# Kernel optimization log

Measured on AMD Instinct MI355X. Metric: run time of the kernel, lower is better.

The kernel has to match this reference:

```python
import jax, jax.numpy as jnp
import numpy as np

B, S, D, H = 8, 1024, 1024, 16
DK = D // H
EPS = 1e-5

def _layernorm(x, w, b):
    mu = jnp.mean(x, axis=-1, keepdims=True)
    var = jnp.mean((x - mu) ** 2, axis=-1, keepdims=True)
    return (x - mu) * jax.lax.rsqrt(var + EPS) * w + b

def setup_inputs() -> dict:
    key = jax.random.key(0)
    ks = jax.random.split(key, 12)
    x = jax.random.normal(ks[0], (B, S, D), dtype=jnp.float32)
    batch_lengths = jax.random.randint(ks[1], (B,), S // 2, S + 1, dtype=jnp.int32)
    sc = 1.0 / np.sqrt(D)
    Wq = jax.random.normal(ks[2], (H, D, DK), dtype=jnp.float32) * sc
    Wk = jax.random.normal(ks[3], (H, D, DK), dtype=jnp.float32) * sc
    Wv = jax.random.normal(ks[4], (H, D, DK), dtype=jnp.float32) * sc
    fc1_w = jax.random.normal(ks[5], (D, D), dtype=jnp.float32) * sc
    fc1_b = jnp.zeros((D,), dtype=jnp.float32)
    fc2_w = jax.random.normal(ks[6], (D, D), dtype=jnp.float32) * sc
    fc2_b = jnp.zeros((D,), dtype=jnp.float32)
    ln1_w = jnp.ones((D,), dtype=jnp.float32)
    ln1_b = jnp.zeros((D,), dtype=jnp.float32)
    ln2_w = jnp.ones((D,), dtype=jnp.float32)
    ln2_b = jnp.zeros((D,), dtype=jnp.float32)
    return {"x": x, "Wq": Wq, "Wk": Wk, "Wv": Wv, "fc1_w": fc1_w, "fc1_b": fc1_b,
            "fc2_w": fc2_w, "fc2_b": fc2_b, "ln1_w": ln1_w, "ln1_b": ln1_b,
            "ln2_w": ln2_w, "ln2_b": ln2_b, "batch_lengths": batch_lengths, "max_len": S}

def reference(x, Wq, Wk, Wv, fc1_w, fc1_b, fc2_w, fc2_b, ln1_w, ln1_b, ln2_w, ln2_b, batch_lengths, max_len):
    b, s, d = x.shape
    h, _, dk = Wq.shape
    # padding masks: valid positions are t < length
    row = (jnp.arange(s)[None, :] < batch_lengths[:, None]).astype(x.dtype)  # [B,S]
    m = row[:, :, None]                 # [B,S,1], outputMask per-row
    mh = m[:, None]                     # [B,1,S,1]
    # all heads batched: Q,K,V -> [B,H,S,dk], masked like Wq(ctx)*mask etc.
    Q = jnp.einsum('bsd,hde->bhse', x, Wq) * mh
    K = jnp.einsum('bsd,hde->bhse', x, Wk) * mh
    V = jnp.einsum('bsd,hde->bhse', x, Wv) * mh
    energy = jnp.einsum('bhqe,bhke->bhqk', Q, K)
    # attnMask: key columns beyond length -> -inf
    key_valid = row[:, None, None, :] > 0
    energy = jnp.where(key_valid, energy, -jnp.inf)
    score = jax.nn.softmax(energy / jnp.sqrt(jnp.asarray(dk, x.dtype)), axis=-1)
    z = jnp.einsum('bhqk,bhke->bhqe', score, V)           # [B,H,S,dk]
    z = z.transpose(0, 2, 1, 3).reshape(b, s, d) * m      # concat heads, mask
    x1 = _layernorm(x + z, ln1_w, ln1_b)
    ff = jax.nn.relu(x1 @ fc1_w + fc1_b) * m
    ff = (ff @ fc2_w + fc2_b) * m
    return _layernorm(x1 + ff, ln2_w, ln2_b)
```

## Files before the change

### kernel.cpp

```cpp
#include <hip/hip_runtime.h>
#include <math.h>

#define B_ 8
#define S_ 1024
#define D_ 1024
#define H_ 16
#define DK_ 64
#define EPS_ 1e-5f

typedef __bf16 bf16_t;
typedef __bf16 bf16x8 __attribute__((ext_vector_type(8)));
typedef __bf16 bf16x4v __attribute__((ext_vector_type(4)));
typedef float  f32x4  __attribute__((ext_vector_type(4)));

__device__ __forceinline__ void gld16(const void* g, void* l) {
    __builtin_amdgcn_global_load_lds(
        (const __attribute__((address_space(1))) void*)g,
        (__attribute__((address_space(3))) void*)l, 16, 0, 0);
}

__global__ __launch_bounds__(256)
void prep(const float* __restrict__ x,
          const float* __restrict__ Wq, const float* __restrict__ Wk,
          const float* __restrict__ Wv, const float* __restrict__ W1,
          const float* __restrict__ W2, bf16_t* __restrict__ xb,
          bf16_t* __restrict__ WtQKV, bf16_t* __restrict__ Wt1,
          bf16_t* __restrict__ Wt2)
{
    __shared__ float tile[64][65];
    const int tid = threadIdx.x;
    const int z = blockIdx.z;

    if (z >= 5) {
        const int blk = (z - 5) * 256 + blockIdx.y * 16 + blockIdx.x;
        const int i = (blk * 256 + tid) * 4;
        const float4 v = *(const float4*)(x + i);
        bf16x4v o = { (bf16_t)v.x, (bf16_t)v.y, (bf16_t)v.z, (bf16_t)v.w };
        *(bf16x4v*)(xb + i) = o;
        return;
    }

    const int n0 = blockIdx.x * 64, k0 = blockIdx.y * 64;
    const int col = tid & 63, r0 = tid >> 6;
    const float* src = (z == 0) ? Wq : (z == 1) ? Wk : (z == 2) ? Wv
                     : (z == 3) ? W1 : W2;
    #pragma unroll
    for (int i = 0; i < 16; i++) {
        const int row = r0 + i * 4;
        float v;
        if (z < 3)
            v = src[((size_t)(n0 >> 6) << 16) + (size_t)(k0 + row) * 64 + col];
        else
            v = src[(size_t)(k0 + row) * D_ + n0 + col];
        tile[row][col] = v;
    }
    __syncthreads();
    bf16_t* dst = (z < 3) ? (WtQKV + (size_t)z * D_ * D_)
                : (z == 3) ? Wt1 : Wt2;
    #pragma unroll
    for (int i = 0; i < 16; i++) {
        const int nr = r0 + i * 4;
        const int n = n0 + nr, k = k0 + col;
        const size_t pidx = ((size_t)(n >> 4) * (D_ >> 3) + (k >> 3)) * 128
                          + (size_t)(n & 15) * 8 + (k & 7);
        dst[pidx] = (bf16_t)tile[col][nr];
    }
}

template<int EPI, typename OUT>
__global__ __launch_bounds__(256, 2)
void gemm_bp(const bf16_t* __restrict__ A, const bf16_t* __restrict__ Bp,
             const float* __restrict__ bias, const int* __restrict__ lens,
             OUT* __restrict__ C, int M, int N, int K)
{
    __shared__ __align__(16) bf16_t As[2][128 * 64];

    const int tid  = threadIdx.x;
    const int lane = tid & 63;
    const int w    = tid >> 6;
    const int quad = lane >> 4, l16 = lane & 15;
    const int wm = w & 1, wn = w >> 1;
    const int sw8 = l16 & 7;

    const int nwg  = gridDim.x * gridDim.y;
    const int orig = blockIdx.y * gridDim.x + blockIdx.x;
    const int swz  = (orig & 7) * (nwg >> 3) + (orig >> 3);
    const int bn = (swz % gridDim.x) * 128;
    const int bm = (swz / gridDim.x) * 128;

    const int rS  = tid >> 3;
    const int cS  = ((tid & 7) ^ (rS & 7)) << 3;
    const int dOf = w * 1024;

    const size_t ntStride = (size_t)(K >> 3) * 128;
    const bf16_t* Bw = Bp + ((size_t)(bn >> 4) + (size_t)wn * 4) * ntStride
                          + (size_t)quad * 128 + (size_t)l16 * 8;

    f32x4 acc[4][4];
    #pragma unroll
    for (int i = 0; i < 4; i++)
        #pragma unroll
        for (int j = 0; j < 4; j++)
            #pragma unroll
            for (int r = 0; r < 4; r++) acc[i][j][r] = 0.f;

#define SA(b_, kt_) { \
    _Pragma("unroll") \
    for (int s_ = 0; s_ < 4; s_++) \
        gld16(A + (size_t)(bm + s_ * 32 + rS) * K + (kt_) * 64 + cS, \
              (char*)As[b_] + s_ * 4096 + dOf); }
#define LB(dst_, kt_) { \
    _Pragma("unroll") \
    for (int j_ = 0; j_ < 4; j_++) \
        _Pragma("unroll") \
        for (int kh_ = 0; kh_ < 2; kh_++) \
            dst_[j_][kh_] = *(const bf16x8*)(Bw + (size_t)j_ * ntStride \
                                             + ((kt_) * 8 + kh_ * 4) * 128); }
#define KSTEP(cb_, nb_, BC_, BX_, t_) { \
    const int ktn_ = ((t_) + 1 < NKT) ? (t_) + 1 : (t_); \
    SA(nb_, ktn_); \
    LB(BX_, ktn_); \
    __builtin_amdgcn_sched_barrier(0); \
    const bf16_t* Ac = As[cb_]; \
    _Pragma("unroll") \
    for (int kh_ = 0; kh_ < 2; kh_++) { \
        bf16x8 a_[4]; \
        _Pragma("unroll") \
        for (int i_ = 0; i_ < 4; i_++) \
            a_[i_] = *(const bf16x8*)&Ac[(wm * 64 + i_ * 16 + l16) * 64 \
                                         + (((kh_ * 4 + quad) ^ sw8) << 3)]; \
        _Pragma("unroll") \
        for (int i_ = 0; i_ < 4; i_++) \
            _Pragma("unroll") \
            for (int j_ = 0; j_ < 4; j_++) \
                acc[i_][j_] = __builtin_amdgcn_mfma_f32_16x16x32_bf16( \
                    a_[i_], BC_[j_][kh_], acc[i_][j_], 0, 0, 0); \
    } \
    __builtin_amdgcn_sched_barrier(0); \
    asm volatile("s_waitcnt vmcnt(8)" ::: "memory"); \
    __builtin_amdgcn_s_barrier(); }

    const int NKT = K >> 6;

    bf16x8 bA[4][2], bB[4][2];
    SA(0, 0);
    LB(bA, 0);
    asm volatile("s_waitcnt vmcnt(8)" ::: "memory");
    __builtin_amdgcn_s_barrier();

    for (int t = 0; t < NKT; t += 2) {
        KSTEP(0, 1, bA, bB, t);
        KSTEP(1, 0, bB, bA, t + 1);
    }

#undef SA
#undef LB
#undef KSTEP

    #pragma unroll
    for (int i = 0; i < 4; i++) {
        #pragma unroll
        for (int r = 0; r < 4; r++) {
            const int m = bm + wm * 64 + i * 16 + quad * 4 + r;
            float keep = 1.f;
            if (EPI != 0) {
                const int s = m & (S_ - 1);
                const int bb = m >> 10;
                keep = (s < lens[bb]) ? 1.f : 0.f;
            }
            #pragma unroll
            for (int j = 0; j < 4; j++) {
                const int n = bn + wn * 64 + j * 16 + l16;
                float v = acc[i][j][r];
                if (EPI != 0) {
                    v += bias[n];
                    if (EPI == 1) v = fmaxf(v, 0.f);
                    v *= keep;
                }
                C[(size_t)m * N + n] = (OUT)v;
            }
        }
    }
}

__global__ __launch_bounds__(256, 3)
void attn_mfma(const bf16_t* __restrict__ QKV, const int* __restrict__ lens,
               bf16_t* __restrict__ Z)
{
    __shared__ __align__(16) bf16_t Ks[2][64][64];
    __shared__ __align__(16) bf16_t Vt[2][64][72];
    __shared__ __align__(16) bf16_t Ps[64][72];

    const int tid  = threadIdx.x;
    const int lane = tid & 63;
    const int w    = tid >> 6;
    const int quad = lane >> 4;
    const int l16  = lane & 15;
    const int id   = blockIdx.x;
    const int b    = id & 7;
    const int h    = (id >> 3) & 15;
    const int qt   = id >> 7;
    const int len  = lens[b];
    const int qbase = qt * 64;
    const bf16_t* Qp = QKV + (size_t)b * S_ * 3072 + (size_t)h * 64;
    const bf16_t* Kp = Qp + 1024;
    const bf16_t* Vp = Qp + 2048;
    const size_t zbase = (size_t)b * S_ * D_ + (size_t)h * 64;

    if (qbase >= len) {
        const int r = tid >> 2, c0 = (tid & 3) * 16;
        bf16_t* zp = Z + zbase + (size_t)(qbase + r) * D_ + c0;
        uint4 zz = {0u, 0u, 0u, 0u};
        *(uint4*)zp = zz;
        *(uint4*)(zp + 8) = zz;
        return;
    }

    const int qrow = qbase + w * 16 + l16;
    const bf16x8 bq0 = *(const bf16x8*)(Qp + (size_t)qrow * 3072 + quad * 8);
    const bf16x8 bq1 = *(const bf16x8*)(Qp + (size_t)qrow * 3072 + 32 + quad * 8);

    const int kr0  = tid >> 3;
    const int kpos = tid & 7;
    const int kc0  = (kpos ^ (kr0 & 7)) << 3;
    const int kc1  = (kpos ^ ((kr0 + 32) & 7)) << 3;

    const int vr  = tid >> 2;
    const int vc0 = (tid & 3) * 16;
    const int vp  = vr ^ ((tid & 3) << 4);

    f32x4 o[4];
    #pragma unroll
    for (int dm = 0; dm < 4; dm++)
        #pragma unroll
        for (int r = 0; r < 4; r++) o[dm][r] = 0.f;
    float l_q = 0.f;

    const int ntiles = (len + 63) >> 6;

    gld16(Kp + (size_t)kr0 * 3072 + kc0,
          (char*)&Ks[0][0][0] + (size_t)(w * 64) * 16);
    gld16(Kp + (size_t)(kr0 + 32) * 3072 + kc1,
          (char*)&Ks[0][0][0] + (size_t)(256 + w * 64) * 16);
    bf16x8 vcur0 = *(const bf16x8*)(Vp + (size_t)vr * 3072 + vc0);
    bf16x8 vcur1 = *(const bf16x8*)(Vp + (size_t)vr * 3072 + vc0 + 8);
    __syncthreads();

    for (int t = 0; t < ntiles; t++) {
        const int k0 = t * 64;
        const int cb = t & 1, nb = (t + 1) & 1;
        const int kn0 = (t + 1 < ntiles ? t + 1 : t) * 64;

        gld16(Kp + (size_t)(kn0 + kr0) * 3072 + kc0,
              (char*)&Ks[nb][0][0] + (size_t)(w * 64) * 16);
        gld16(Kp + (size_t)(kn0 + kr0 + 32) * 3072 + kc1,
              (char*)&Ks[nb][0][0] + (size_t)(256 + w * 64) * 16);
        const bf16_t* vsrc = Vp + (size_t)(kn0 + vr) * 3072 + vc0;
        const bf16x8 vn0 = *(const bf16x8*)vsrc;
        const bf16x8 vn1 = *(const bf16x8*)(vsrc + 8);
        __builtin_amdgcn_sched_barrier(0);

        #pragma unroll
        for (int kt = 0; kt < 4; kt++) {
            const int r = kt * 16 + l16;
            const bf16x8 ak0 = *(const bf16x8*)&Ks[cb][r][(quad ^ (l16 & 7)) << 3];
            const bf16x8 ak1 = *(const bf16x8*)&Ks[cb][r][((4 + quad) ^ (l16 & 7)) << 3];
            f32x4 z4 = {0.f, 0.f, 0.f, 0.f};
            z4 = __builtin_amdgcn_mfma_f32_16x16x32_bf16(ak0, bq0, z4, 0, 0, 0);
            const f32x4 sfv = __builtin_amdgcn_mfma_f32_16x16x32_bf16(ak1, bq1, z4, 0, 0, 0);
            bf16x4v pk;
            #pragma unroll
            for (int r2 = 0; r2 < 4; r2++) {
                const int key = k0 + kt * 16 + quad * 4 + r2;
                float p = __expf(sfv[r2] * 0.125f);
                p = (key < len) ? p : 0.f;
                l_q += p;
                pk[r2] = (bf16_t)p;
            }
            *(bf16x4v*)&Ps[w * 16 + l16][kt * 16 + quad * 4] = pk;
        }

        #pragma unroll
        for (int i = 0; i < 8; i++) Vt[cb][vc0 + i][vp] = vcur0[i];
        #pragma unroll
        for (int i = 0; i < 8; i++) Vt[cb][vc0 + 8 + i][vp] = vcur1[i];
        vcur0 = vn0;
        vcur1 = vn1;
        __syncthreads();

        const bf16x8 bp0 = *(const bf16x8*)&Ps[w * 16 + l16][quad * 8];
        const bf16x8 bp1 = *(const bf16x8*)&Ps[w * 16 + l16][32 + quad * 8];
        #pragma unroll
        for (int dm = 0; dm < 4; dm++) {
            const bf16x8 av0 = *(const bf16x8*)&Vt[cb][dm * 16 + l16][(quad * 8) ^ (dm * 16)];
            const bf16x8 av1 = *(const bf16x8*)&Vt[cb][dm * 16 + l16][(32 + quad * 8) ^ (dm * 16)];
            o[dm] = __builtin_amdgcn_mfma_f32_16x16x32_bf16(av0, bp0, o[dm], 0, 0, 0);
            o[dm] = __builtin_amdgcn_mfma_f32_16x16x32_bf16(av1, bp1, o[dm], 0, 0, 0);
        }
    }

    l_q += __shfl_xor(l_q, 16);
    l_q += __shfl_xor(l_q, 32);
    const int qg = qbase + w * 16 + l16;
    const float inv = (qg < len) ? 1.f / l_q : 0.f;
    bf16_t* zrow = Z + zbase + (size_t)qg * D_;
    #pragma unroll
    for (int dm = 0; dm < 4; dm++) {
        bf16x4v st;
        #pragma unroll
        for (int r = 0; r < 4; r++) st[r] = (bf16_t)(o[dm][r] * inv);
        *(bf16x4v*)(zrow + dm * 16 + quad * 4) = st;
    }
}

__device__ __forceinline__ void ln_core(float vx, float vy, float vz, float vw,
                                        int tid, float& mean, float& rstd)
{
    __shared__ float red[8];
    float s = vx + vy + vz + vw;
    #pragma unroll
    for (int off = 32; off; off >>= 1) s += __shfl_xor(s, off, 64);
    const int wv = tid >> 6, lane = tid & 63;
    if (lane == 0) red[wv] = s;
    __syncthreads();
    mean = (red[0] + red[1] + red[2] + red[3]) * (1.f / D_);
    const float dx = vx - mean, dy = vy - mean, dz = vz - mean, dw = vw - mean;
    float s2 = dx * dx + dy * dy + dz * dz + dw * dw;
    #pragma unroll
    for (int off = 32; off; off >>= 1) s2 += __shfl_xor(s2, off, 64);
    if (lane == 0) red[4 + wv] = s2;
    __syncthreads();
    rstd = rsqrtf((red[4] + red[5] + red[6] + red[7]) * (1.f / D_) + EPS_);
}

__global__ __launch_bounds__(256)
void add_ln1(const float* __restrict__ X, const bf16_t* __restrict__ Y,
             const float* __restrict__ g, const float* __restrict__ beta,
             bf16_t* __restrict__ out)
{
    const int row = blockIdx.x, tid = threadIdx.x;
    const float4 xv = ((const float4*)(X + (size_t)row * D_))[tid];
    const bf16x4v yv = *(const bf16x4v*)(Y + (size_t)row * D_ + tid * 4);
    const float vx = xv.x + (float)yv[0], vy = xv.y + (float)yv[1];
    const float vz = xv.z + (float)yv[2], vw = xv.w + (float)yv[3];
    float mean, rstd;
    ln_core(vx, vy, vz, vw, tid, mean, rstd);
    const float4 gv = ((const float4*)g)[tid];
    const float4 bv = ((const float4*)beta)[tid];
    bf16x4v o;
    o[0] = (bf16_t)((vx - mean) * rstd * gv.x + bv.x);
    o[1] = (bf16_t)((vy - mean) * rstd * gv.y + bv.y);
    o[2] = (bf16_t)((vz - mean) * rstd * gv.z + bv.z);
    o[3] = (bf16_t)((vw - mean) * rstd * gv.w + bv.w);
    *(bf16x4v*)(out + (size_t)row * D_ + tid * 4) = o;
}

__global__ __launch_bounds__(256)
void add_ln2(const bf16_t* __restrict__ X, const float* __restrict__ Y,
             const float* __restrict__ g, const float* __restrict__ beta,
             float* __restrict__ out)
{
    const int row = blockIdx.x, tid = threadIdx.x;
    const bf16x4v xv = *(const bf16x4v*)(X + (size_t)row * D_ + tid * 4);
    const float4 yv = ((const float4*)(Y + (size_t)row * D_))[tid];
    const float vx = (float)xv[0] + yv.x, vy = (float)xv[1] + yv.y;
    const float vz = (float)xv[2] + yv.z, vw = (float)xv[3] + yv.w;
    float mean, rstd;
    ln_core(vx, vy, vz, vw, tid, mean, rstd);
    const float4 gv = ((const float4*)g)[tid];
    const float4 bv = ((const float4*)beta)[tid];
    float4 o;
    o.x = (vx - mean) * rstd * gv.x + bv.x;
    o.y = (vy - mean) * rstd * gv.y + bv.y;
    o.z = (vz - mean) * rstd * gv.z + bv.z;
    o.w = (vw - mean) * rstd * gv.w + bv.w;
    ((float4*)(out + (size_t)row * D_))[tid] = o;
}

extern "C" void kernel_launch(void* const* d_in, const int* in_sizes, int n_in,
                              void* d_out, int out_size, void* d_ws, size_t ws_size,
                              hipStream_t stream)
{
    const float* x    = (const float*)d_in[0];
    const float* Wq   = (const float*)d_in[1];
    const float* Wk   = (const float*)d_in[2];
    const float* Wv   = (const float*)d_in[3];
    const float* fc1w = (const float*)d_in[4];
    const float* fc1b = (const float*)d_in[5];
    const float* fc2w = (const float*)d_in[6];
    const float* fc2b = (const float*)d_in[7];
    const float* ln1w = (const float*)d_in[8];
    const float* ln1b = (const float*)d_in[9];
    const float* ln2w = (const float*)d_in[10];
    const float* ln2b = (const float*)d_in[11];
    const int*   lens = (const int*)d_in[12];
    float* out = (float*)d_out;

    char* ws = (char*)d_ws;
    const size_t MB = 1024 * 1024;
    bf16_t* QKVb  = (bf16_t*)(ws);
    bf16_t* Zb    = (bf16_t*)(ws + 48 * MB);
    bf16_t* X1b   = (bf16_t*)(ws + 80 * MB);
    bf16_t* xb    = (bf16_t*)(ws + 96 * MB);
    bf16_t* H1b   = (bf16_t*)(ws + 96 * MB);
    float*  FF    = (float*)(ws + 48 * MB);
    bf16_t* WtQKV = (bf16_t*)(ws + 112 * MB);
    bf16_t* Wt1   = (bf16_t*)(ws + 118 * MB);
    bf16_t* Wt2   = (bf16_t*)(ws + 120 * MB);

    const int M = B_ * S_;

    prep<<<dim3(16, 16, 37), 256, 0, stream>>>(x, Wq, Wk, Wv, fc1w, fc2w,
                                               xb, WtQKV, Wt1, Wt2);

    gemm_bp<0, bf16_t><<<dim3(3072 / 128, M / 128), 256, 0, stream>>>(
        xb, WtQKV, nullptr, nullptr, QKVb, M, 3072, D_);

    attn_mfma<<<dim3(2048), 256, 0, stream>>>(QKVb, lens, Zb);

    add_ln1<<<M, 256, 0, stream>>>(x, Zb, ln1w, ln1b, X1b);

    gemm_bp<1, bf16_t><<<dim3(D_ / 128, M / 128), 256, 0, stream>>>(
        X1b, Wt1, fc1b, lens, H1b, M, D_, D_);
    gemm_bp<2, float><<<dim3(D_ / 128, M / 128), 256, 0, stream>>>(
        H1b, Wt2, fc2b, lens, FF, M, D_, D_);

    add_ln2<<<M, 256, 0, stream>>>(X1b, FF, ln2w, ln2b, out);
}
```

Baseline: 310.6 us.

## Double attention query tile to 128 rows with 512-thread blocks sharing K/V tiles

The attention kernel now handles 128 query rows per block with 8 waves instead of 64 rows with 4 waves, and launches half as many blocks. Each staged K/V tile in LDS is reused by twice as many queries, roughly halving global K/V traffic per query. Per-thread load work is redistributed so each thread moves one 16-byte K chunk and one 8-element V chunk. In exchange, blocks are larger, the query-tile early exit is coarser (more padded work for partially valid tiles), and occupancy and scheduling change.

```diff
diff --git a/kernel.cpp b/kernel.cpp
--- a/kernel.cpp
+++ b/kernel.cpp
@@ -183,13 +183,13 @@
     }
 }
 
-__global__ __launch_bounds__(256, 3)
+__global__ __launch_bounds__(512, 4)
 void attn_mfma(const bf16_t* __restrict__ QKV, const int* __restrict__ lens,
                bf16_t* __restrict__ Z)
 {
     __shared__ __align__(16) bf16_t Ks[2][64][64];
     __shared__ __align__(16) bf16_t Vt[2][64][72];
-    __shared__ __align__(16) bf16_t Ps[64][72];
+    __shared__ __align__(16) bf16_t Ps[128][72];
 
     const int tid  = threadIdx.x;
     const int lane = tid & 63;
@@ -201,7 +201,7 @@
     const int h    = (id >> 3) & 15;
     const int qt   = id >> 7;
     const int len  = lens[b];
-    const int qbase = qt * 64;
+    const int qbase = qt * 128;
     const bf16_t* Qp = QKV + (size_t)b * S_ * 3072 + (size_t)h * 64;
     const bf16_t* Kp = Qp + 1024;
     const bf16_t* Vp = Qp + 2048;
@@ -220,14 +220,13 @@
     const bf16x8 bq0 = *(const bf16x8*)(Qp + (size_t)qrow * 3072 + quad * 8);
     const bf16x8 bq1 = *(const bf16x8*)(Qp + (size_t)qrow * 3072 + 32 + quad * 8);
 
-    const int kr0  = tid >> 3;
-    const int kpos = tid & 7;
-    const int kc0  = (kpos ^ (kr0 & 7)) << 3;
-    const int kc1  = (kpos ^ ((kr0 + 32) & 7)) << 3;
-
-    const int vr  = tid >> 2;
-    const int vc0 = (tid & 3) * 16;
-    const int vp  = vr ^ ((tid & 3) << 4);
+    const int kr = tid >> 3;
+    const int kc = ((tid & 7) ^ (kr & 7)) << 3;
+
+    const int vr  = tid >> 3;
+    const int cg8 = tid & 7;
+    const int vc0 = cg8 * 8;
+    const int vp  = vr ^ ((cg8 >> 1) << 4);
 
     f32x4 o[4];
     #pragma unroll
@@ -238,12 +237,8 @@
 
     const int ntiles = (len + 63) >> 6;
 
-    gld16(Kp + (size_t)kr0 * 3072 + kc0,
-          (char*)&Ks[0][0][0] + (size_t)(w * 64) * 16);
-    gld16(Kp + (size_t)(kr0 + 32) * 3072 + kc1,
-          (char*)&Ks[0][0][0] + (size_t)(256 + w * 64) * 16);
-    bf16x8 vcur0 = *(const bf16x8*)(Vp + (size_t)vr * 3072 + vc0);
-    bf16x8 vcur1 = *(const bf16x8*)(Vp + (size_t)vr * 3072 + vc0 + 8);
+    gld16(Kp + (size_t)kr * 3072 + kc, (char*)&Ks[0][0][0] + w * 1024);
+    bf16x8 vcur = *(const bf16x8*)(Vp + (size_t)vr * 3072 + vc0);
     __syncthreads();
 
     for (int t = 0; t < ntiles; t++) {
@@ -251,13 +246,8 @@
         const int cb = t & 1, nb = (t + 1) & 1;
         const int kn0 = (t + 1 < ntiles ? t + 1 : t) * 64;
 
-        gld16(Kp + (size_t)(kn0 + kr0) * 3072 + kc0,
-              (char*)&Ks[nb][0][0] + (size_t)(w * 64) * 16);
-        gld16(Kp + (size_t)(kn0 + kr0 + 32) * 3072 + kc1,
-              (char*)&Ks[nb][0][0] + (size_t)(256 + w * 64) * 16);
-        const bf16_t* vsrc = Vp + (size_t)(kn0 + vr) * 3072 + vc0;
-        const bf16x8 vn0 = *(const bf16x8*)vsrc;
-        const bf16x8 vn1 = *(const bf16x8*)(vsrc + 8);
+        gld16(Kp + (size_t)(kn0 + kr) * 3072 + kc, (char*)&Ks[nb][0][0] + w * 1024);
+        const bf16x8 vn = *(const bf16x8*)(Vp + (size_t)(kn0 + vr) * 3072 + vc0);
         __builtin_amdgcn_sched_barrier(0);
 
         #pragma unroll
@@ -281,11 +271,8 @@
         }
 
         #pragma unroll
-        for (int i = 0; i < 8; i++) Vt[cb][vc0 + i][vp] = vcur0[i];
-        #pragma unroll
-        for (int i = 0; i < 8; i++) Vt[cb][vc0 + 8 + i][vp] = vcur1[i];
-        vcur0 = vn0;
-        vcur1 = vn1;
+        for (int i = 0; i < 8; i++) Vt[cb][vc0 + i][vp] = vcur[i];
+        vcur = vn;
         __syncthreads();
 
         const bf16x8 bp0 = *(const bf16x8*)&Ps[w * 16 + l16][quad * 8];
@@ -416,7 +403,7 @@
     gemm_bp<0, bf16_t><<<dim3(3072 / 128, M / 128), 256, 0, stream>>>(
         xb, WtQKV, nullptr, nullptr, QKVb, M, 3072, D_);
 
-    attn_mfma<<<dim3(2048), 256, 0, stream>>>(QKVb, lens, Zb);
+    attn_mfma<<<dim3(1024), 512, 0, stream>>>(QKVb, lens, Zb);
 
     add_ln1<<<M, 256, 0, stream>>>(x, Zb, ln1w, ln1b, X1b);
 
```

Measured after the change: 305.4 us. About the same (-1.7%).
